# Optimization experiments

Hardware: AMD Instinct MI355X
Metric: run time of the kernel (lower is better)

Reference implementation:

```python
import jax, jax.numpy as jnp
import numpy as np

B, T = 128, 128
CONT, HID, EMB = 16, 128, 64
K, CE, VSP, VLC = 8192, 6, 2000, 32
BETA = 0.25
FUSE_IN = 3 * HID  # naip_rep + cont_h + cat_h, each HID wide


def setup_inputs() -> dict:
    key = jax.random.key(0)
    ks = jax.random.split(key, 40)

    def w(i, shape):
        return jax.random.normal(ks[i], shape, dtype=jnp.float32) * 0.05

    return {
        'cont': jax.random.normal(ks[0], (B, T, CONT), dtype=jnp.float32),
        'naip': jax.random.normal(ks[1], (B, 1, 3, 3), dtype=jnp.float32),
        'cat': jax.random.randint(ks[2], (B, T, 2), 0, VLC, dtype=jnp.int32),
        # encoder params
        'cat_emb_sp': w(3, (VSP, CE)),
        'cat_emb_lc': w(4, (VLC, CE)),
        'conv_w': w(5, (HID, 1, 3, 3)), 'conv_b': w(6, (HID,)),
        'naip_proj_w': w(7, (HID, HID)), 'naip_proj_b': w(8, (HID,)),
        'cont_proj_w': w(9, (HID, CONT)), 'cont_proj_b': w(10, (HID,)),
        'cat_proj_w': w(11, (HID, 2 * CE)), 'cat_proj_b': w(12, (HID,)),
        'fuse1_w': w(13, (HID, FUSE_IN)), 'fuse1_b': w(14, (HID,)),
        'fuse2_w': w(15, (EMB, HID)), 'fuse2_b': w(16, (EMB,)),
        # quantizer
        'codebook': w(17, (K, EMB)),
        # decoder params
        'bb1_w': w(18, (HID, EMB)), 'bb1_b': w(19, (HID,)),
        'bb2_w': w(20, (HID, HID)), 'bb2_b': w(21, (HID,)),
        'cont_head_w': w(22, (CONT, HID)), 'cont_head_b': w(23, (CONT,)),
        'sp_head_w': w(24, (VSP, HID)), 'sp_head_b': w(25, (VSP,)),
        'lc_head_w': w(26, (VLC, HID)), 'lc_head_b': w(27, (VLC,)),
        'can1_w': w(28, (HID, HID)), 'can1_b': w(29, (HID,)),
        'can2_w': w(30, (1, HID)), 'can2_b': w(31, (1,)),
    }


def lin(x, w, b):
    return x @ w.T + b


def reference(cont, naip, cat, cat_emb_sp, cat_emb_lc, conv_w, conv_b,
              naip_proj_w, naip_proj_b, cont_proj_w, cont_proj_b,
              cat_proj_w, cat_proj_b, fuse1_w, fuse1_b, fuse2_w, fuse2_b,
              codebook, bb1_w, bb1_b, bb2_w, bb2_b, cont_head_w, cont_head_b,
              sp_head_w, sp_head_b, lc_head_w, lc_head_b,
              can1_w, can1_b, can2_w, can2_b):
    # ---- encoder ----
    naip = jnp.nan_to_num(naip, nan=0.0, posinf=0.0, neginf=0.0)
    # Conv2d(k=3) on a 3x3 patch == full contraction -> [B, HID]
    naip_feat = jax.nn.relu(jnp.einsum('bchw,ochw->bo', naip, conv_w) + conv_b)
    naip_feat = lin(naip_feat, naip_proj_w, naip_proj_b)          # [B, HID]
    naip_rep = jnp.broadcast_to(naip_feat[:, None, :], (B, T, HID))

    cont_h = lin(jnp.nan_to_num(cont, nan=0.0, posinf=0.0, neginf=0.0),
                 cont_proj_w, cont_proj_b)                        # [B, T, HID]

    cat_concat = jnp.concatenate([cat_emb_sp[cat[..., 0]],
                                  cat_emb_lc[cat[..., 1]]], axis=-1)  # [B,T,2*CE]
    cat_h = lin(cat_concat, cat_proj_w, cat_proj_b)               # [B, T, HID]

    fused = jnp.concatenate([naip_rep, cont_h, cat_h], axis=-1)   # [B, T, 3*HID]
    z_e = lin(jax.nn.relu(lin(fused, fuse1_w, fuse1_b)), fuse2_w, fuse2_b)  # [B,T,EMB]

    # ---- ST vector quantizer ----
    z = z_e.reshape(-1, EMB)                                       # [N, EMB]
    z_sq = jnp.sum(z * z, axis=1, keepdims=True)                   # [N, 1]
    e_sq = jnp.sum(codebook * codebook, axis=1)                    # [K]
    distances = z_sq + e_sq[None, :] - 2.0 * (z @ codebook.T)      # [N, K]
    indices = jnp.argmin(distances, axis=1)                        # [N]
    z_q = codebook[indices].reshape(z_e.shape)                     # [B, T, EMB]

    commitment = jnp.mean((jax.lax.stop_gradient(z_e) - z_q) ** 2)
    codebook_l = jnp.mean((z_e - jax.lax.stop_gradient(z_q)) ** 2)
    loss_vq = codebook_l + BETA * commitment
    z_q_st = z_e + jax.lax.stop_gradient(z_q - z_e)

    counts = jnp.bincount(indices, length=K).astype(jnp.float32)
    avg_probs = counts / indices.shape[0]
    perplexity = jnp.exp(-jnp.sum(avg_probs * jnp.log(avg_probs + 1e-12)))

    # ---- decoder ----
    h = jax.nn.relu(lin(jax.nn.relu(lin(z_q_st, bb1_w, bb1_b)), bb2_w, bb2_b))  # [B,T,HID]
    cont_rec = lin(h, cont_head_w, cont_head_b)                    # [B, T, CONT]
    sp_logits = lin(h, sp_head_w, sp_head_b)                       # [B, T, VSP]
    lc_logits = lin(h, lc_head_w, lc_head_b)                       # [B, T, VLC]
    h_last = h[:, -1, :]
    canopy = jnp.squeeze(lin(jax.nn.relu(lin(h_last, can1_w, can1_b)), can2_w, can2_b), -1)  # [B]

    return (cont_rec, sp_logits, lc_logits, canopy,
            indices.reshape(B, T), loss_vq, perplexity)
```

## Files before the change

kernel.cpp:

```cpp
#include <hip/hip_runtime.h>
#include <cmath>

namespace {
constexpr int Bn = 128, Tn = 128, BTn = Bn * Tn;
constexpr int CONTn = 16, HIDn = 128, EMBn = 64;
constexpr int Kn = 8192, CEn = 6, VSPn = 2000, VLCn = 32, FINn = 3 * HIDn;
constexpr int VSP_PAD = 2048;
constexpr int CAP = 128;
constexpr float EPSC = 0.02f;
constexpr int TOKB = 32;
constexpr int KCW = 64;
constexpr int NIT = Kn / (KCW * 8);

constexpr size_t WS_NAIP2 = 0;
constexpr size_t WS_ZE    = WS_NAIP2 + (size_t)Bn * HIDn;
constexpr size_t WS_ZQ    = WS_ZE + (size_t)BTn * EMBn;
constexpr size_t WS_H     = WS_ZQ + (size_t)BTn * EMBn;
constexpr size_t WS_ESQ   = WS_H + (size_t)BTn * HIDn;
constexpr size_t WS_PART  = WS_ESQ + Kn;
constexpr size_t WS_CNTK  = WS_PART + BTn / 4;
constexpr size_t WS_CNTT  = WS_CNTK + Kn;
constexpr size_t WS_Q     = WS_CNTT + BTn;
constexpr size_t WS_CAND  = WS_Q + BTn;
constexpr size_t WS_ZBF   = WS_CAND + (size_t)BTn * CAP;
constexpr size_t WS_CBBF  = WS_ZBF + (size_t)BTn * EMBn / 2;
constexpr size_t WS_HBF   = WS_CBBF + (size_t)Kn * EMBn / 2;
constexpr size_t WS_WBF   = WS_HBF + (size_t)BTn * HIDn / 2;
constexpr size_t WS_RCG   = WS_WBF + (size_t)VSP_PAD * HIDn / 2;

constexpr size_t O_CONT = 0;
constexpr size_t O_SP   = O_CONT + (size_t)BTn * CONTn;
constexpr size_t O_LC   = O_SP + (size_t)BTn * VSPn;
constexpr size_t O_CAN  = O_LC + (size_t)BTn * VLCn;
constexpr size_t O_IDX  = O_CAN + Bn;
constexpr size_t O_LOSS = O_IDX + BTn;
constexpr size_t O_PPL  = O_LOSS + 1;
}

typedef __attribute__((ext_vector_type(8))) short short8v;
typedef __attribute__((ext_vector_type(4))) float f32x4;

__device__ __forceinline__ float nan0(float v) {
    return __builtin_isfinite(v) ? v : 0.0f;
}
__device__ __forceinline__ float dot4(float4 a, float4 b) {
    return a.x * b.x + a.y * b.y + a.z * b.z + a.w * b.w;
}
__device__ __forceinline__ unsigned short f2bf(float f) {
    union { float f; unsigned u; } v{f};
    unsigned r = v.u + 0x7FFFu + ((v.u >> 16) & 1u);
    return (unsigned short)(r >> 16);
}
__device__ __forceinline__ unsigned fenc(float f) {
    unsigned b = __float_as_uint(f);
    return (b & 0x80000000u) ? ~b : (b | 0x80000000u);
}
__device__ __forceinline__ float fdec(unsigned k) {
    unsigned b = (k >> 31) ? (k & 0x7fffffffu) : ~k;
    return __uint_as_float(b);
}

__global__ __launch_bounds__(256) void k_esq_zero(const float* __restrict__ cb,
                                                  float* __restrict__ e_sq,
                                                  int* __restrict__ counts,
                                                  unsigned short* __restrict__ cbbf) {
    int i = blockIdx.x * 256 + threadIdx.x;
    if (i < Kn) {
        counts[i] = 0;
        const float4* r = (const float4*)(cb + (size_t)i * EMBn);
        float s = 0.f;
#pragma unroll
        for (int j = 0; j < 16; ++j) {
            float4 v = r[j];
            s += dot4(v, v);
            unsigned short u[4] = {f2bf(v.x), f2bf(v.y), f2bf(v.z), f2bf(v.w)};
            *(uint2*)(cbbf + (size_t)i * EMBn + j * 4) = *(const uint2*)u;
        }
        e_sq[i] = s;
    }
}

__global__ __launch_bounds__(256) void k_rcmax(const float* __restrict__ e_sq,
                                               float* __restrict__ rcg) {
    const int tid = threadIdx.x;
    float m = 0.f;
#pragma unroll
    for (int j = 0; j < Kn / 256; ++j) m = fmaxf(m, e_sq[j * 256 + tid]);
#pragma unroll
    for (int off = 32; off > 0; off >>= 1) m = fmaxf(m, __shfl_xor(m, off));
    __shared__ float wm[4];
    if ((tid & 63) == 0) wm[tid >> 6] = m;
    __syncthreads();
    if (tid == 0)
        rcg[0] = sqrtf(fmaxf(fmaxf(wm[0], wm[1]), fmaxf(wm[2], wm[3]))) * 1.000001f;
}

__global__ __launch_bounds__(256) void k_wcast(const float* __restrict__ w,
                                               unsigned short* __restrict__ wbf) {
    int i = blockIdx.x * 256 + threadIdx.x;
    int v = i >> 5;
    unsigned short u[4] = {0, 0, 0, 0};
    if (v < VSPn) {
        float4 x = ((const float4*)w)[i];
        u[0] = f2bf(x.x); u[1] = f2bf(x.y); u[2] = f2bf(x.z); u[3] = f2bf(x.w);
    }
    *(uint2*)(wbf + (size_t)i * 4) = *(const uint2*)u;
}

__global__ __launch_bounds__(128) void k_naip(const float* __restrict__ naip,
                                              const float* __restrict__ conv_w,
                                              const float* __restrict__ conv_b,
                                              const float* __restrict__ pw,
                                              const float* __restrict__ pb,
                                              float* __restrict__ naip2) {
    int b = blockIdx.x, o = threadIdx.x;
    __shared__ float feat[HIDn];
    float acc = conv_b[o];
#pragma unroll
    for (int i = 0; i < 9; ++i) acc += nan0(naip[b * 9 + i]) * conv_w[o * 9 + i];
    feat[o] = fmaxf(acc, 0.f);
    __syncthreads();
    float a2 = pb[o];
    const float4* wr = (const float4*)(pw + (size_t)o * HIDn);
    const float4* fr = (const float4*)feat;
#pragma unroll
    for (int j = 0; j < 32; ++j) a2 += dot4(fr[j], wr[j]);
    naip2[(size_t)b * HIDn + o] = a2;
}

__global__ __launch_bounds__(256) void k_ze(
    const float* __restrict__ cont, const int* __restrict__ cat,
    const float* __restrict__ emb_sp, const float* __restrict__ emb_lc,
    const float* __restrict__ cpw, const float* __restrict__ cpb,
    const float* __restrict__ caw, const float* __restrict__ cab,
    const float* __restrict__ f1w, const float* __restrict__ f1b,
    const float* __restrict__ f2w, const float* __restrict__ f2b,
    const float* __restrict__ naip2, float* __restrict__ z_e) {
    const int tok0 = blockIdx.x * 16;
    const int tid = threadIdx.x;
    __shared__ float fused[16][FINn + 4];
    __shared__ float h1[16][HIDn + 4];

    for (int idx = tid; idx < 16 * HIDn; idx += 256) {
        int t = idx >> 7, j = idx & 127;
        int b = (tok0 + t) / Tn;
        fused[t][j] = naip2[(size_t)b * HIDn + j];
    }
    for (int idx = tid; idx < 16 * HIDn; idx += 256) {
        int t = idx >> 7, o = idx & 127;
        int tok = tok0 + t;
        const float4* cp = (const float4*)(cont + (size_t)tok * CONTn);
        const float4* wr = (const float4*)(cpw + (size_t)o * CONTn);
        float a = cpb[o];
#pragma unroll
        for (int q = 0; q < 4; ++q) {
            float4 c4 = cp[q], w4 = wr[q];
            a += nan0(c4.x) * w4.x + nan0(c4.y) * w4.y + nan0(c4.z) * w4.z + nan0(c4.w) * w4.w;
        }
        fused[t][HIDn + o] = a;
    }
    for (int idx = tid; idx < 16 * HIDn; idx += 256) {
        int t = idx >> 7, o = idx & 127;
        int tok = tok0 + t;
        int c0 = cat[tok * 2], c1 = cat[tok * 2 + 1];
        const float* e0 = emb_sp + (size_t)c0 * CEn;
        const float* e1 = emb_lc + (size_t)c1 * CEn;
        const float* wr = caw + (size_t)o * (2 * CEn);
        float a = cab[o];
#pragma unroll
        for (int i = 0; i < CEn; ++i) a += e0[i] * wr[i];
#pragma unroll
        for (int i = 0; i < CEn; ++i) a += e1[i] * wr[CEn + i];
        fused[t][2 * HIDn + o] = a;
    }
    __syncthreads();
    {
        int o = tid >> 1, half = tid & 1;
        float acc[8];
        float bv = f1b[o];
#pragma unroll
        for (int t = 0; t < 8; ++t) acc[t] = bv;
        const float4* wr = (const float4*)(f1w + (size_t)o * FINn);
        for (int kk = 0; kk < FINn / 4; ++kk) {
            float4 w = wr[kk];
#pragma unroll
            for (int t = 0; t < 8; ++t) {
                float4 f = ((const float4*)&fused[half * 8 + t][0])[kk];
                acc[t] += dot4(f, w);
            }
        }
#pragma unroll
        for (int t = 0; t < 8; ++t) h1[half * 8 + t][o] = fmaxf(acc[t], 0.f);
    }
    __syncthreads();
    {
        int o = tid & 63, tg = tid >> 6;
        float acc[4];
        float bv = f2b[o];
#pragma unroll
        for (int t = 0; t < 4; ++t) acc[t] = bv;
        const float4* wr = (const float4*)(f2w + (size_t)o * HIDn);
        for (int kk = 0; kk < HIDn / 4; ++kk) {
            float4 w = wr[kk];
#pragma unroll
            for (int t = 0; t < 4; ++t) {
                float4 f = ((const float4*)&h1[tg * 4 + t][0])[kk];
                acc[t] += dot4(f, w);
            }
        }
#pragma unroll
        for (int t = 0; t < 4; ++t) z_e[(size_t)(tok0 + tg * 4 + t) * EMBn + o] = acc[t];
    }
}

__global__ __launch_bounds__(256) void k_zprep(const float* __restrict__ z_e,
                                               unsigned short* __restrict__ zbf,
                                               float* __restrict__ qtok) {
    const int lane = threadIdx.x & 63;
    const int tg = threadIdx.x >> 6;
    const int t = blockIdx.x * 4 + tg;
    float zv = z_e[(size_t)t * EMBn + lane];
    zbf[(size_t)t * EMBn + lane] = f2bf(zv);
    float s = zv * zv;
#pragma unroll
    for (int off = 32; off > 0; off >>= 1) s += __shfl_xor(s, off);
    if (lane == 0) qtok[t] = EPSC * sqrtf(s);
}

__global__ __launch_bounds__(512, 4) void k_vq_sweep(
    const unsigned short* __restrict__ zbf, const unsigned short* __restrict__ cbbf,
    const float* __restrict__ e_sq, const float* __restrict__ qtok,
    const float* __restrict__ rcg,
    int* __restrict__ cntT, int* __restrict__ cand) {
    const int tid = threadIdx.x;
    const int lane = tid & 63;
    const int wid = tid >> 6;
    const int lrow = lane & 15;
    const int g = lane >> 4;
    const int tok0 = blockIdx.x * TOKB;

    __shared__ unsigned tauL[TOKB];
    __shared__ int cntL[TOKB];
    if (tid < TOKB) { tauL[tid] = 0u; cntL[tid] = 0; }

    short8v bz[2][2];
#pragma unroll
    for (int n = 0; n < 2; ++n)
#pragma unroll
        for (int kc = 0; kc < 2; ++kc)
            bz[n][kc] = *(const short8v*)(zbf + (size_t)(tok0 + n * 16 + lrow) * EMBn + kc * 32 + g * 8);
    float qn[2];
#pragma unroll
    for (int n = 0; n < 2; ++n) qn[n] = qtok[tok0 + n * 16 + lrow];
    const float rcm = rcg[0];
    __syncthreads();

    for (int it = 0; it < NIT; ++it) {
        const int c0 = (it * 8 + wid) * KCW;
        short8v ac[4][2];
        float4 e4[4];
#pragma unroll
        for (int m = 0; m < 4; ++m) {
#pragma unroll
            for (int kc = 0; kc < 2; ++kc)
                ac[m][kc] = *(const short8v*)(cbbf + (size_t)(c0 + m * 16 + lrow) * EMBn + kc * 32 + g * 8);
            e4[m] = *(const float4*)(e_sq + c0 + m * 16 + g * 4);
        }
        f32x4 acc[4][2];
#pragma unroll
        for (int m = 0; m < 4; ++m) {
            f32x4 em = {-0.5f * e4[m].x, -0.5f * e4[m].y, -0.5f * e4[m].z, -0.5f * e4[m].w};
            acc[m][0] = em;
            acc[m][1] = em;
        }
#pragma unroll
        for (int kc = 0; kc < 2; ++kc)
#pragma unroll
            for (int m = 0; m < 4; ++m)
#pragma unroll
                for (int n = 0; n < 2; ++n)
                    acc[m][n] = __builtin_amdgcn_mfma_f32_16x16x32_bf16(ac[m][kc], bz[n][kc], acc[m][n], 0, 0, 0);

#pragma unroll
        for (int n = 0; n < 2; ++n) {
            float v = acc[0][n][0];
#pragma unroll
            for (int m = 0; m < 4; ++m)
#pragma unroll
                for (int r = 0; r < 4; ++r) v = fmaxf(v, acc[m][n][r]);
            v = fmaxf(v, __shfl_xor(v, 16));
            v = fmaxf(v, __shfl_xor(v, 32));
            if (lane < 16) atomicMax(&tauL[n * 16 + lane], fenc(v));
            float tf = fmaxf(fdec(tauL[n * 16 + lrow]), v);
            float nthr = tf - qn[n] * rcm;
            const int tn = n * 16 + lrow;
#pragma unroll
            for (int m = 0; m < 4; ++m)
#pragma unroll
                for (int r = 0; r < 4; ++r)
                    if (acc[m][n][r] >= nthr) {
                        int slot = atomicAdd(&cntL[tn], 1);
                        if (slot < CAP)
                            cand[(size_t)(tok0 + tn) * CAP + slot] = c0 + m * 16 + g * 4 + r;
                    }
        }
    }
    __syncthreads();
    if (tid < TOKB) cntT[tok0 + tid] = cntL[tid];
}

__global__ __launch_bounds__(256) void k_vq_rescore(
    const int* __restrict__ cntT, const int* __restrict__ cand,
    const float* __restrict__ z_e, const float* __restrict__ cb,
    const float* __restrict__ e_sq,
    float* __restrict__ z_q, float* __restrict__ idx_out,
    int* __restrict__ counts, float* __restrict__ partials) {
    const int lane = threadIdx.x & 63;
    const int tg = threadIdx.x >> 6;
    const int t = blockIdx.x * 4 + tg;
    __shared__ float psum[4];

    float4 z[16];
    const float4* zr = (const float4*)(z_e + (size_t)t * EMBn);
#pragma unroll
    for (int q = 0; q < 16; ++q) z[q] = zr[q];

    const int n = cntT[t];
    float best = INFINITY;
    int bi = Kn;

    if (n > 0 && n <= CAP) {
        for (int s = lane; s < n; s += 64) {
            int c = cand[(size_t)t * CAP + s];
            const float4* cp = (const float4*)(cb + (size_t)c * EMBn);
            float a = 0.f;
#pragma unroll
            for (int q = 0; q < 16; ++q) a += dot4(z[q], cp[q]);
            float d = e_sq[c] - 2.f * a;
            if (d < best || (d == best && c < bi)) { best = d; bi = c; }
        }
    } else {
        for (int c0 = 0; c0 < Kn; c0 += 64) {
            int c = c0 + lane;
            const float4* cp = (const float4*)(cb + (size_t)c * EMBn);
            float a = 0.f;
#pragma unroll
            for (int q = 0; q < 16; ++q) a += dot4(z[q], cp[q]);
            float d = e_sq[c] - 2.f * a;
            if (d < best) { best = d; bi = c; }
        }
    }
#pragma unroll
    for (int off = 32; off > 0; off >>= 1) {
        float od = __shfl_xor(best, off);
        int oi = __shfl_xor(bi, off);
        if (od < best || (od == best && oi < bi)) { best = od; bi = oi; }
    }

    float cv = cb[(size_t)bi * EMBn + lane];
    z_q[(size_t)t * EMBn + lane] = cv;
    float zv = z_e[(size_t)t * EMBn + lane];
    float diff = zv - cv;
    float s = diff * diff;
#pragma unroll
    for (int off = 32; off > 0; off >>= 1) s += __shfl_xor(s, off);
    if (lane == 0) {
        psum[tg] = s;
        idx_out[t] = (float)bi;
        atomicAdd(&counts[bi], 1);
    }
    __syncthreads();
    if (threadIdx.x == 0) partials[blockIdx.x] = psum[0] + psum[1] + psum[2] + psum[3];
}

__global__ __launch_bounds__(256) void k_backbone(
    const float* __restrict__ z_q,
    const float* __restrict__ bb1w, const float* __restrict__ bb1b,
    const float* __restrict__ bb2w, const float* __restrict__ bb2b,
    const float* __restrict__ chw, const float* __restrict__ chb,
    const float* __restrict__ lcw, const float* __restrict__ lcb,
    float* __restrict__ h_out, unsigned short* __restrict__ hbf_out,
    float* __restrict__ cont_rec, float* __restrict__ lc_out) {
    const int tid = threadIdx.x;
    const int tok0 = blockIdx.x * 16;
    __shared__ float zq[16][68];
    __shared__ float h1[16][HIDn + 4];
    __shared__ float h2[16][HIDn + 4];
    {
        int t = tid >> 4, q = tid & 15;
        ((float4*)&zq[t][0])[q] = ((const float4*)(z_q + (size_t)(tok0 + t) * EMBn))[q];
    }
    __syncthreads();
    {
        int o = tid >> 1, half = tid & 1;
        float acc[8];
        float bv = bb1b[o];
#pragma unroll
        for (int t = 0; t < 8; ++t) acc[t] = bv;
        const float4* wr = (const float4*)(bb1w + (size_t)o * EMBn);
#pragma unroll
        for (int kk = 0; kk < 16; ++kk) {
            float4 w = wr[kk];
#pragma unroll
            for (int t = 0; t < 8; ++t) acc[t] += dot4(((const float4*)&zq[half * 8 + t][0])[kk], w);
        }
#pragma unroll
        for (int t = 0; t < 8; ++t) h1[half * 8 + t][o] = fmaxf(acc[t], 0.f);
    }
    __syncthreads();
    {
        int o = tid >> 1, half = tid & 1;
        float acc[8];
        float bv = bb2b[o];
#pragma unroll
        for (int t = 0; t < 8; ++t) acc[t] = bv;
        const float4* wr = (const float4*)(bb2w + (size_t)o * HIDn);
        for (int kk = 0; kk < 32; ++kk) {
            float4 w = wr[kk];
#pragma unroll
            for (int t = 0; t < 8; ++t) acc[t] += dot4(((const float4*)&h1[half * 8 + t][0])[kk], w);
        }
#pragma unroll
        for (int t = 0; t < 8; ++t) {
            float v = fmaxf(acc[t], 0.f);
            h2[half * 8 + t][o] = v;
            h_out[(size_t)(tok0 + half * 8 + t) * HIDn + o] = v;
            hbf_out[(size_t)(tok0 + half * 8 + t) * HIDn + o] = f2bf(v);
        }
    }
    __syncthreads();
    {
        int t = tid >> 4, o = tid & 15;
        float a = chb[o];
        const float4* wr = (const float4*)(chw + (size_t)o * HIDn);
#pragma unroll
        for (int kk = 0; kk < 32; ++kk) a += dot4(((const float4*)&h2[t][0])[kk], wr[kk]);
        cont_rec[(size_t)(tok0 + t) * CONTn + o] = a;
    }
    for (int idx = tid; idx < 16 * 32; idx += 256) {
        int t = idx >> 5, o = idx & 31;
        float a = lcb[o];
        const float4* wr = (const float4*)(lcw + (size_t)o * HIDn);
#pragma unroll
        for (int kk = 0; kk < 32; ++kk) a += dot4(((const float4*)&h2[t][0])[kk], wr[kk]);
        lc_out[(size_t)(tok0 + t) * VLCn + o] = a;
    }
}

__global__ __launch_bounds__(256, 3) void k_sp_mfma(
    const unsigned short* __restrict__ hbf, const unsigned short* __restrict__ wbf,
    const float* __restrict__ bias, float* __restrict__ out) {
    const int tid = threadIdx.x;
    const int lane = tid & 63;
    const int wid = tid >> 6;
    const int tok_w = blockIdx.y * 128 + (wid & 1) * 64;
    const int v_w = blockIdx.x * 128 + (wid >> 1) * 64;

    const int lrow = lane & 15;
    const int lk = (lane >> 4) * 8;

    const unsigned short* ha = hbf + (size_t)(tok_w + lrow) * HIDn + lk;
    const unsigned short* wa = wbf + (size_t)(v_w + lrow) * HIDn + lk;

    f32x4 acc[4][4];
#pragma unroll
    for (int m = 0; m < 4; ++m)
#pragma unroll
        for (int n = 0; n < 4; ++n) acc[m][n] = (f32x4){0.f, 0.f, 0.f, 0.f};

#pragma unroll
    for (int ks = 0; ks < 4; ++ks) {
        const int kk = ks * 32;
        short8v a[4], b[4];
#pragma unroll
        for (int m = 0; m < 4; ++m)
            a[m] = *(const short8v*)(ha + (size_t)m * 16 * HIDn + kk);
#pragma unroll
        for (int n = 0; n < 4; ++n)
            b[n] = *(const short8v*)(wa + (size_t)n * 16 * HIDn + kk);
#pragma unroll
        for (int m = 0; m < 4; ++m)
#pragma unroll
            for (int n = 0; n < 4; ++n)
                acc[m][n] = __builtin_amdgcn_mfma_f32_16x16x32_bf16(a[m], b[n], acc[m][n], 0, 0, 0);
    }

    const int r0 = (lane >> 4) * 4;
#pragma unroll
    for (int n = 0; n < 4; ++n) {
        const int col = v_w + n * 16 + lrow;
        if (col < VSPn) {
            const float bv = bias[col];
#pragma unroll
            for (int m = 0; m < 4; ++m) {
                const int row = tok_w + m * 16 + r0;
#pragma unroll
                for (int r = 0; r < 4; ++r)
                    out[(size_t)(row + r) * VSPn + col] = acc[m][n][r] + bv;
            }
        }
    }
}

__global__ __launch_bounds__(128) void k_canopy(const float* __restrict__ h,
                                                const float* __restrict__ w1,
                                                const float* __restrict__ b1,
                                                const float* __restrict__ w2,
                                                const float* __restrict__ b2,
                                                float* __restrict__ can) {
    int b = blockIdx.x, o = threadIdx.x;
    __shared__ float r[128];
    const float4* hr = (const float4*)(h + (size_t)(b * Tn + Tn - 1) * HIDn);
    const float4* wr = (const float4*)(w1 + (size_t)o * HIDn);
    float a = b1[o];
#pragma unroll
    for (int kk = 0; kk < 32; ++kk) a += dot4(hr[kk], wr[kk]);
    r[o] = fmaxf(a, 0.f) * w2[o];
    __syncthreads();
    for (int s = 64; s > 0; s >>= 1) {
        if (o < s) r[o] += r[o + s];
        __syncthreads();
    }
    if (o == 0) can[b] = r[0] + b2[0];
}

__global__ __launch_bounds__(256) void k_finalize(const float* __restrict__ partials,
                                                  const int* __restrict__ counts,
                                                  float* __restrict__ out_loss,
                                                  float* __restrict__ out_ppl) {
    const int tid = threadIdx.x;
    __shared__ float red[256];
    float ps = 0.f;
#pragma unroll
    for (int j = 0; j < (BTn / 4) / 256; ++j) ps += partials[tid * ((BTn / 4) / 256) + j];
    red[tid] = ps;
    __syncthreads();
    for (int s = 128; s > 0; s >>= 1) {
        if (tid < s) red[tid] += red[tid + s];
        __syncthreads();
    }
    float total = red[0];
    __syncthreads();
    float e = 0.f;
    for (int i = tid; i < Kn; i += 256) {
        float p = (float)counts[i] * (1.0f / BTn);
        e += p * logf(p + 1e-12f);
    }
    red[tid] = e;
    __syncthreads();
    for (int s = 128; s > 0; s >>= 1) {
        if (tid < s) red[tid] += red[tid + s];
        __syncthreads();
    }
    if (tid == 0) {
        out_loss[0] = 1.25f * total / (float)((size_t)BTn * EMBn);
        out_ppl[0] = expf(-red[0]);
    }
}

extern "C" void kernel_launch(void* const* d_in, const int* in_sizes, int n_in,
                              void* d_out, int out_size, void* d_ws, size_t ws_size,
                              hipStream_t stream) {
    const float* cont = (const float*)d_in[0];
    const float* naip = (const float*)d_in[1];
    const int* cat = (const int*)d_in[2];
    const float* emb_sp = (const float*)d_in[3];
    const float* emb_lc = (const float*)d_in[4];
    const float* conv_w = (const float*)d_in[5];
    const float* conv_b = (const float*)d_in[6];
    const float* npw = (const float*)d_in[7];
    const float* npb = (const float*)d_in[8];
    const float* cpw = (const float*)d_in[9];
    const float* cpb = (const float*)d_in[10];
    const float* caw = (const float*)d_in[11];
    const float* cab = (const float*)d_in[12];
    const float* f1w = (const float*)d_in[13];
    const float* f1b = (const float*)d_in[14];
    const float* f2w = (const float*)d_in[15];
    const float* f2b = (const float*)d_in[16];
    const float* cb = (const float*)d_in[17];
    const float* bb1w = (const float*)d_in[18];
    const float* bb1b = (const float*)d_in[19];
    const float* bb2w = (const float*)d_in[20];
    const float* bb2b = (const float*)d_in[21];
    const float* chw = (const float*)d_in[22];
    const float* chb = (const float*)d_in[23];
    const float* spw = (const float*)d_in[24];
    const float* spb = (const float*)d_in[25];
    const float* lcw = (const float*)d_in[26];
    const float* lcb = (const float*)d_in[27];
    const float* c1w = (const float*)d_in[28];
    const float* c1b = (const float*)d_in[29];
    const float* c2w = (const float*)d_in[30];
    const float* c2b = (const float*)d_in[31];

    float* out = (float*)d_out;
    float* ws = (float*)d_ws;
    float* naip2 = ws + WS_NAIP2;
    float* z_e = ws + WS_ZE;
    float* z_q = ws + WS_ZQ;
    float* h = ws + WS_H;
    float* e_sq = ws + WS_ESQ;
    float* parts = ws + WS_PART;
    int* counts = (int*)(ws + WS_CNTK);
    int* cntT = (int*)(ws + WS_CNTT);
    float* qtok = ws + WS_Q;
    int* cand = (int*)(ws + WS_CAND);
    unsigned short* zbf = (unsigned short*)(ws + WS_ZBF);
    unsigned short* cbbf = (unsigned short*)(ws + WS_CBBF);
    unsigned short* hbf = (unsigned short*)(ws + WS_HBF);
    unsigned short* wbf = (unsigned short*)(ws + WS_WBF);
    float* rcg = ws + WS_RCG;

    k_esq_zero<<<dim3(Kn / 256), dim3(256), 0, stream>>>(cb, e_sq, counts, cbbf);
    k_rcmax<<<dim3(1), dim3(256), 0, stream>>>(e_sq, rcg);
    k_wcast<<<dim3(VSP_PAD * HIDn / 4 / 256), dim3(256), 0, stream>>>(spw, wbf);
    k_naip<<<dim3(Bn), dim3(128), 0, stream>>>(naip, conv_w, conv_b, npw, npb, naip2);
    k_ze<<<dim3(BTn / 16), dim3(256), 0, stream>>>(cont, cat, emb_sp, emb_lc, cpw, cpb, caw, cab,
                                                   f1w, f1b, f2w, f2b, naip2, z_e);
    k_zprep<<<dim3(BTn / 4), dim3(256), 0, stream>>>(z_e, zbf, qtok);
    k_vq_sweep<<<dim3(BTn / TOKB), dim3(512), 0, stream>>>(zbf, cbbf, e_sq, qtok, rcg, cntT, cand);
    k_vq_rescore<<<dim3(BTn / 4), dim3(256), 0, stream>>>(cntT, cand, z_e, cb, e_sq, z_q,
                                                          out + O_IDX, counts, parts);
    k_backbone<<<dim3(BTn / 16), dim3(256), 0, stream>>>(z_q, bb1w, bb1b, bb2w, bb2b, chw, chb,
                                                         lcw, lcb, h, hbf, out + O_CONT, out + O_LC);
    k_sp_mfma<<<dim3(VSP_PAD / 128, BTn / 128), dim3(256), 0, stream>>>(hbf, wbf, spb, out + O_SP);
    k_canopy<<<dim3(Bn), dim3(128), 0, stream>>>(h, c1w, c1b, c2w, c2b, out + O_CAN);
    k_finalize<<<dim3(1), dim3(256), 0, stream>>>(parts, counts, out + O_LOSS, out + O_PPL);
}
```

Measured before the change: 309.2 us.

## Split encoder into fused-build, tiled fuse1 GEMM, and fuse2 kernels

Breaks the monolithic encoder kernel into three kernels: one writes the concatenated fused features to global memory, one runs fuse1 as a 64-token by 128-output register-blocked GEMM with swizzled LDS tiles, and one runs fuse2. The old fuse1 path streamed the full weight row from global memory for every 16-token block with little reuse. The new GEMM stages weights in shared memory and reuses them across 64 tokens. In exchange it adds two launches and a global round-trip for the fused and h1 intermediates.

```diff
diff --git a/kernel.cpp b/kernel.cpp
--- a/kernel.cpp
+++ b/kernel.cpp
@@ -27,6 +27,8 @@
 constexpr size_t WS_HBF   = WS_CBBF + (size_t)Kn * EMBn / 2;
 constexpr size_t WS_WBF   = WS_HBF + (size_t)BTn * HIDn / 2;
 constexpr size_t WS_RCG   = WS_WBF + (size_t)VSP_PAD * HIDn / 2;
+constexpr size_t WS_FUSED = WS_RCG + 1;
+constexpr size_t WS_H1    = WS_FUSED + (size_t)BTn * FINn;
 
 constexpr size_t O_CONT = 0;
 constexpr size_t O_SP   = O_CONT + (size_t)BTn * CONTn;
@@ -128,25 +130,20 @@
     naip2[(size_t)b * HIDn + o] = a2;
 }
 
-__global__ __launch_bounds__(256) void k_ze(
+__global__ __launch_bounds__(256) void k_fused(
     const float* __restrict__ cont, const int* __restrict__ cat,
     const float* __restrict__ emb_sp, const float* __restrict__ emb_lc,
     const float* __restrict__ cpw, const float* __restrict__ cpb,
     const float* __restrict__ caw, const float* __restrict__ cab,
-    const float* __restrict__ f1w, const float* __restrict__ f1b,
-    const float* __restrict__ f2w, const float* __restrict__ f2b,
-    const float* __restrict__ naip2, float* __restrict__ z_e) {
-    const int tok0 = blockIdx.x * 16;
-    const int tid = threadIdx.x;
-    __shared__ float fused[16][FINn + 4];
-    __shared__ float h1[16][HIDn + 4];
-
-    for (int idx = tid; idx < 16 * HIDn; idx += 256) {
+    const float* __restrict__ naip2, float* __restrict__ fused_g) {
+    const int tok0 = blockIdx.x * 64;
+    const int tid = threadIdx.x;
+    for (int idx = tid; idx < 64 * HIDn; idx += 256) {
         int t = idx >> 7, j = idx & 127;
-        int b = (tok0 + t) / Tn;
-        fused[t][j] = naip2[(size_t)b * HIDn + j];
-    }
-    for (int idx = tid; idx < 16 * HIDn; idx += 256) {
+        int tok = tok0 + t;
+        fused_g[(size_t)tok * FINn + j] = naip2[(size_t)(tok >> 7) * HIDn + j];
+    }
+    for (int idx = tid; idx < 64 * HIDn; idx += 256) {
         int t = idx >> 7, o = idx & 127;
         int tok = tok0 + t;
         const float4* cp = (const float4*)(cont + (size_t)tok * CONTn);
@@ -157,9 +154,9 @@
             float4 c4 = cp[q], w4 = wr[q];
             a += nan0(c4.x) * w4.x + nan0(c4.y) * w4.y + nan0(c4.z) * w4.z + nan0(c4.w) * w4.w;
         }
-        fused[t][HIDn + o] = a;
-    }
-    for (int idx = tid; idx < 16 * HIDn; idx += 256) {
+        fused_g[(size_t)tok * FINn + HIDn + o] = a;
+    }
+    for (int idx = tid; idx < 64 * HIDn; idx += 256) {
         int t = idx >> 7, o = idx & 127;
         int tok = tok0 + t;
         int c0 = cat[tok * 2], c1 = cat[tok * 2 + 1];
@@ -171,46 +168,99 @@
         for (int i = 0; i < CEn; ++i) a += e0[i] * wr[i];
 #pragma unroll
         for (int i = 0; i < CEn; ++i) a += e1[i] * wr[CEn + i];
-        fused[t][2 * HIDn + o] = a;
-    }
-    __syncthreads();
-    {
-        int o = tid >> 1, half = tid & 1;
-        float acc[8];
-        float bv = f1b[o];
-#pragma unroll
-        for (int t = 0; t < 8; ++t) acc[t] = bv;
-        const float4* wr = (const float4*)(f1w + (size_t)o * FINn);
-        for (int kk = 0; kk < FINn / 4; ++kk) {
-            float4 w = wr[kk];
-#pragma unroll
-            for (int t = 0; t < 8; ++t) {
-                float4 f = ((const float4*)&fused[half * 8 + t][0])[kk];
-                acc[t] += dot4(f, w);
+        fused_g[(size_t)tok * FINn + 2 * HIDn + o] = a;
+    }
+}
+
+__global__ __launch_bounds__(256, 4) void k_f1(const float* __restrict__ fused_g,
+                                               const float* __restrict__ f1w,
+                                               const float* __restrict__ f1b,
+                                               float* __restrict__ h1g) {
+    const int tid = threadIdx.x;
+    const int x = tid & 15, y = tid >> 4;
+    const int tok0 = blockIdx.x * 64;
+    __shared__ __align__(16) float ht[64 * 32];
+    __shared__ __align__(16) float wt[128 * 32];
+
+    float acc[4][8];
+#pragma unroll
+    for (int j = 0; j < 8; ++j) {
+        float bv = f1b[x + 16 * j];
+#pragma unroll
+        for (int t = 0; t < 4; ++t) acc[t][j] = bv;
+    }
+
+    for (int s = 0; s < 12; ++s) {
+        __syncthreads();
+#pragma unroll
+        for (int w = 0; w < 2; ++w) {
+            int idx = tid + w * 256;
+            int row = idx >> 3, c4 = idx & 7;
+            float4 v = *(const float4*)(fused_g + (size_t)(tok0 + row) * FINn + s * 32 + c4 * 4);
+            ((float4*)ht)[row * 8 + (c4 ^ ((row >> 2) & 3))] = v;
+        }
+#pragma unroll
+        for (int w = 0; w < 4; ++w) {
+            int idx = tid + w * 256;
+            int row = idx >> 3, c4 = idx & 7;
+            float4 v = *(const float4*)(f1w + (size_t)row * FINn + s * 32 + c4 * 4);
+            ((float4*)wt)[row * 8 + (c4 ^ (row & 7))] = v;
+        }
+        __syncthreads();
+#pragma unroll
+        for (int kk = 0; kk < 8; ++kk) {
+            float4 hh[4], ww[8];
+#pragma unroll
+            for (int t = 0; t < 4; ++t) {
+                int row = y * 4 + t;
+                hh[t] = ((const float4*)ht)[row * 8 + (kk ^ ((row >> 2) & 3))];
             }
-        }
-#pragma unroll
-        for (int t = 0; t < 8; ++t) h1[half * 8 + t][o] = fmaxf(acc[t], 0.f);
-    }
-    __syncthreads();
-    {
-        int o = tid & 63, tg = tid >> 6;
-        float acc[4];
-        float bv = f2b[o];
-#pragma unroll
-        for (int t = 0; t < 4; ++t) acc[t] = bv;
-        const float4* wr = (const float4*)(f2w + (size_t)o * HIDn);
-        for (int kk = 0; kk < HIDn / 4; ++kk) {
-            float4 w = wr[kk];
-#pragma unroll
-            for (int t = 0; t < 4; ++t) {
-                float4 f = ((const float4*)&h1[tg * 4 + t][0])[kk];
-                acc[t] += dot4(f, w);
+#pragma unroll
+            for (int j = 0; j < 8; ++j) {
+                int row = x + 16 * j;
+                ww[j] = ((const float4*)wt)[row * 8 + (kk ^ (row & 7))];
             }
-        }
-#pragma unroll
-        for (int t = 0; t < 4; ++t) z_e[(size_t)(tok0 + tg * 4 + t) * EMBn + o] = acc[t];
-    }
+#pragma unroll
+            for (int t = 0; t < 4; ++t)
+#pragma unroll
+                for (int j = 0; j < 8; ++j) acc[t][j] += dot4(hh[t], ww[j]);
+        }
+    }
+#pragma unroll
+    for (int t = 0; t < 4; ++t)
+#pragma unroll
+        for (int j = 0; j < 8; ++j)
+            h1g[(size_t)(tok0 + y * 4 + t) * HIDn + x + 16 * j] = fmaxf(acc[t][j], 0.f);
+}
+
+__global__ __launch_bounds__(256) void k_f2(const float* __restrict__ h1g,
+                                            const float* __restrict__ f2w,
+                                            const float* __restrict__ f2b,
+                                            float* __restrict__ z_e) {
+    const int tok0 = blockIdx.x * 16;
+    const int tid = threadIdx.x;
+    __shared__ float h1[16][HIDn + 4];
+    for (int idx = tid; idx < 16 * 32; idx += 256) {
+        int t = idx >> 5, q = idx & 31;
+        ((float4*)&h1[t][0])[q] = ((const float4*)(h1g + (size_t)(tok0 + t) * HIDn))[q];
+    }
+    __syncthreads();
+    int o = tid & 63, tg = tid >> 6;
+    float acc[4];
+    float bv = f2b[o];
+#pragma unroll
+    for (int t = 0; t < 4; ++t) acc[t] = bv;
+    const float4* wr = (const float4*)(f2w + (size_t)o * HIDn);
+    for (int kk = 0; kk < HIDn / 4; ++kk) {
+        float4 w = wr[kk];
+#pragma unroll
+        for (int t = 0; t < 4; ++t) {
+            float4 f = ((const float4*)&h1[tg * 4 + t][0])[kk];
+            acc[t] += dot4(f, w);
+        }
+    }
+#pragma unroll
+    for (int t = 0; t < 4; ++t) z_e[(size_t)(tok0 + tg * 4 + t) * EMBn + o] = acc[t];
 }
 
 __global__ __launch_bounds__(256) void k_zprep(const float* __restrict__ z_e,
@@ -611,13 +661,17 @@
     unsigned short* hbf = (unsigned short*)(ws + WS_HBF);
     unsigned short* wbf = (unsigned short*)(ws + WS_WBF);
     float* rcg = ws + WS_RCG;
+    float* fused_g = ws + WS_FUSED;
+    float* h1g = ws + WS_H1;
 
     k_esq_zero<<<dim3(Kn / 256), dim3(256), 0, stream>>>(cb, e_sq, counts, cbbf);
     k_rcmax<<<dim3(1), dim3(256), 0, stream>>>(e_sq, rcg);
     k_wcast<<<dim3(VSP_PAD * HIDn / 4 / 256), dim3(256), 0, stream>>>(spw, wbf);
     k_naip<<<dim3(Bn), dim3(128), 0, stream>>>(naip, conv_w, conv_b, npw, npb, naip2);
-    k_ze<<<dim3(BTn / 16), dim3(256), 0, stream>>>(cont, cat, emb_sp, emb_lc, cpw, cpb, caw, cab,
-                                                   f1w, f1b, f2w, f2b, naip2, z_e);
+    k_fused<<<dim3(BTn / 64), dim3(256), 0, stream>>>(cont, cat, emb_sp, emb_lc, cpw, cpb,
+                                                      caw, cab, naip2, fused_g);
+    k_f1<<<dim3(BTn / 64), dim3(256), 0, stream>>>(fused_g, f1w, f1b, h1g);
+    k_f2<<<dim3(BTn / 16), dim3(256), 0, stream>>>(h1g, f2w, f2b, z_e);
     k_zprep<<<dim3(BTn / 4), dim3(256), 0, stream>>>(z_e, zbf, qtok);
     k_vq_sweep<<<dim3(BTn / TOKB), dim3(512), 0, stream>>>(zbf, cbbf, e_sq, qtok, rcg, cntT, cand);
     k_vq_rescore<<<dim3(BTn / 4), dim3(256), 0, stream>>>(cntT, cand, z_e, cb, e_sq, z_q,
```

After: 719.8 us. 2.33x slower.
